# Kernel optimization log

Measured on AMD Instinct MI355X. Metric: run time of the kernel, lower is better.

The kernel has to match this reference:

```python
import jax, jax.numpy as jnp
import numpy as np

N_NODES = 50000
N_EDGES = 400000
IN, HID, OUT = 256, 64, 64
HEADS = (8, 8, 1)
NEG_SLOPE = 0.2


def setup_inputs() -> dict:
    key = jax.random.key(0)
    ks = jax.random.split(key, 16)
    def lin(k, fi, fo):
        return jax.random.normal(k, (fi, fo), jnp.float32) / np.sqrt(fi)
    H0, H1, H2 = HEADS
    return {
        "x": jax.random.normal(ks[0], (N_NODES, IN), jnp.float32),
        "src": jax.random.randint(ks[1], (N_EDGES,), 0, N_NODES),
        "dst": jax.random.randint(ks[2], (N_EDGES,), 0, N_NODES),
        # layer 0: in=256 -> (8 heads, 64)
        "W1": lin(ks[3], IN, H0 * HID),
        "al1": 0.1 * jax.random.normal(ks[4], (H0, HID), jnp.float32),
        "ar1": 0.1 * jax.random.normal(ks[5], (H0, HID), jnp.float32),
        "b1": jnp.zeros((H0 * HID,), jnp.float32),
        # layer 1: in=512 -> (8 heads, 64), identity residual (512 == 8*64)
        "W2": lin(ks[6], H0 * HID, H1 * HID),
        "al2": 0.1 * jax.random.normal(ks[7], (H1, HID), jnp.float32),
        "ar2": 0.1 * jax.random.normal(ks[8], (H1, HID), jnp.float32),
        "b2": jnp.zeros((H1 * HID,), jnp.float32),
        # layer 2: in=512 -> (1 head, 64), linear residual projection
        "W3": lin(ks[9], H1 * HID, H2 * OUT),
        "al3": 0.1 * jax.random.normal(ks[10], (H2, OUT), jnp.float32),
        "ar3": 0.1 * jax.random.normal(ks[11], (H2, OUT), jnp.float32),
        "b3": jnp.zeros((H2 * OUT,), jnp.float32),
        "Wr3": lin(ks[12], H1 * HID, H2 * OUT),
    }


def _gat_conv(h, src, dst, W, al, ar, b, res, act):
    # DGL GATConv on a homogeneous graph (feat_src == feat_dst).
    N = h.shape[0]
    H, D = al.shape
    f = (h @ W).reshape(N, H, D)                       # [N,H,D]
    el = jnp.sum(f * al[None], axis=-1)                # [N,H]
    er = jnp.sum(f * ar[None], axis=-1)                # [N,H]
    e = jax.nn.leaky_relu(el[src] + er[dst], NEG_SLOPE)  # [E,H]
    # segment softmax over incoming edges of each dst node
    m = jax.ops.segment_max(e, dst, num_segments=N)    # [N,H]
    ex = jnp.exp(e - m[dst])
    denom = jax.ops.segment_sum(ex, dst, num_segments=N)
    alpha = ex / denom[dst]                            # [E,H]
    msg = f[src] * alpha[:, :, None]                   # [E,H,D]
    rst = jax.ops.segment_sum(msg, dst, num_segments=N)  # [N,H,D]
    if res is not None:
        rst = rst + res
    rst = rst + b.reshape(1, H, D)
    return act(rst) if act is not None else rst


def reference(x, src, dst, W1, al1, ar1, b1, W2, al2, ar2, b2,
              W3, al3, ar3, b3, Wr3):
    N = x.shape[0]
    h = _gat_conv(x, src, dst, W1, al1, ar1, b1, None, jax.nn.elu)
    h = h.reshape(N, -1)                               # flatten(1)
    res2 = h.reshape(N, HEADS[1], HID)                 # identity residual
    h = _gat_conv(h, src, dst, W2, al2, ar2, b2, res2, jax.nn.elu)
    h = h.reshape(N, -1)
    res3 = (h @ Wr3).reshape(N, HEADS[2], OUT)         # projected residual
    h = _gat_conv(h, src, dst, W3, al3, ar3, b3, res3, None)
    return h.mean(axis=1)                              # mean over heads
```

## Files before the change

kernel.cpp:

```cpp
#include <hip/hip_runtime.h>
#include <hip/hip_bf16.h>

#define N_NODES 50000
#define M_PAD 50048
#define N_EDGES 400000
#define SCAN_B 256

typedef __attribute__((ext_vector_type(8))) short short8;
typedef __attribute__((ext_vector_type(4))) float f32x4;

__device__ __forceinline__ float b2f(unsigned short u) {
    return __uint_as_float(((unsigned)u) << 16);
}
__device__ __forceinline__ unsigned short f2b(float f) {
    unsigned u = __float_as_uint(f);
    return (unsigned short)((u + 0x7fffu + ((u >> 16) & 1u)) >> 16);
}
__device__ __forceinline__ float blo(unsigned u) { return __uint_as_float(u << 16); }
__device__ __forceinline__ float bhi(unsigned u) { return __uint_as_float(u & 0xffff0000u); }

__device__ __forceinline__ void gload_lds16(const void* g, void* l) {
    __builtin_amdgcn_global_load_lds(
        (const __attribute__((address_space(1))) unsigned int*)g,
        (__attribute__((address_space(3))) unsigned int*)l, 16, 0, 0);
}

__global__ __launch_bounds__(256) void conv_x4(const float* __restrict__ x,
                                               unsigned short* __restrict__ xb, int n4) {
    int i = blockIdx.x * blockDim.x + threadIdx.x;
    if (i >= n4) return;
    float4 v = *(const float4*)&x[(size_t)i * 4];
    unsigned short o[4] = {f2b(v.x), f2b(v.y), f2b(v.z), f2b(v.w)};
    *(ushort2*)&xb[(size_t)i * 4] = make_ushort2(o[0], o[1]);
    *(ushort2*)&xb[(size_t)i * 4 + 2] = make_ushort2(o[2], o[3]);
}

#define W1_SZ (512 * 256)
#define W2_SZ (512 * 512)
#define W3_SZ (64 * 512)
__global__ __launch_bounds__(256) void conv_wt_all(const float* __restrict__ W1,
                                                   const float* __restrict__ W2,
                                                   const float* __restrict__ W3,
                                                   const float* __restrict__ Wr3,
                                                   unsigned short* __restrict__ Wt1,
                                                   unsigned short* __restrict__ Wt2,
                                                   unsigned short* __restrict__ Wt3) {
    int o = blockIdx.x * blockDim.x + threadIdx.x;
    if (o < W1_SZ) {
        int n = o / 256, k = o % 256;
        Wt1[o] = f2b(W1[(size_t)k * 512 + n]);
    } else if (o < W1_SZ + W2_SZ) {
        int oo = o - W1_SZ;
        int n = oo / 512, k = oo % 512;
        Wt2[oo] = f2b(W2[(size_t)k * 512 + n]);
    } else if (o < W1_SZ + W2_SZ + W3_SZ) {
        int oo = o - W1_SZ - W2_SZ;
        int n = oo / 512, k = oo % 512;
        Wt3[oo] = f2b(W3[(size_t)k * 64 + n]);
    } else if (o < W1_SZ + W2_SZ + 2 * W3_SZ) {
        int oo = o - W1_SZ - W2_SZ - W3_SZ;
        int n = oo / 512, k = oo % 512;
        Wt3[W3_SZ + oo] = f2b(Wr3[(size_t)k * 64 + n]);
    }
}

template <int H, bool ELER>
__global__ __launch_bounds__(256, 2) void gemm_mfma(const unsigned short* __restrict__ A,
                                                    const unsigned short* __restrict__ Bt,
                                                    unsigned short* __restrict__ C,
                                                    const float* __restrict__ al,
                                                    const float* __restrict__ ar,
                                                    float* __restrict__ el,
                                                    float* __restrict__ er,
                                                    int M, int NN, int K) {
    __shared__ unsigned short As[128 * 32];
    __shared__ unsigned short Bs[128 * 32];
    const int tid = threadIdx.x;
    const int w = tid >> 6, l = tid & 63;
    const int bm = blockIdx.y * 128, bn = blockIdx.x * 128;
    const int wr = w >> 1, wc = w & 1;
    const int rA = l >> 2;
    const int kA = (l & 3) * 8;
    const int fr = l & 15, fq = l >> 4;
    f32x4 acc[4][4] = {};

    for (int k0 = 0; k0 < K; k0 += 32) {
#pragma unroll
        for (int j = 0; j < 2; ++j) {
            int row = w * 32 + j * 16 + rA;
            gload_lds16(&A[(size_t)(bm + row) * K + k0 + kA], &As[(w * 2 + j) * 512]);
            gload_lds16(&Bt[(size_t)(bn + row) * K + k0 + kA], &Bs[(w * 2 + j) * 512]);
        }
        __syncthreads();
        short8 a[4], b[4];
#pragma unroll
        for (int m = 0; m < 4; ++m)
            a[m] = *(const short8*)&As[(wr * 64 + m * 16 + fr) * 32 + fq * 8];
#pragma unroll
        for (int n = 0; n < 4; ++n)
            b[n] = *(const short8*)&Bs[(wc * 64 + n * 16 + fr) * 32 + fq * 8];
#pragma unroll
        for (int m = 0; m < 4; ++m)
#pragma unroll
            for (int n = 0; n < 4; ++n)
                acc[m][n] = __builtin_amdgcn_mfma_f32_16x16x32_bf16(a[m], b[n], acc[m][n], 0, 0, 0);
        __syncthreads();
    }

    if (ELER) {
        const int head = (bn >> 6) + wc;
        if (head < H) {
            float alv[4], arv[4];
#pragma unroll
            for (int n = 0; n < 4; ++n) {
                alv[n] = al[head * 64 + n * 16 + fr];
                arv[n] = ar[head * 64 + n * 16 + fr];
            }
#pragma unroll
            for (int m = 0; m < 4; ++m) {
#pragma unroll
                for (int j = 0; j < 4; ++j) {
                    float pl = acc[m][0][j] * alv[0] + acc[m][1][j] * alv[1] +
                               acc[m][2][j] * alv[2] + acc[m][3][j] * alv[3];
                    float pr = acc[m][0][j] * arv[0] + acc[m][1][j] * arv[1] +
                               acc[m][2][j] * arv[2] + acc[m][3][j] * arv[3];
#pragma unroll
                    for (int off = 1; off < 16; off <<= 1) {
                        pl += __shfl_xor(pl, off);
                        pr += __shfl_xor(pr, off);
                    }
                    int r = bm + wr * 64 + m * 16 + fq * 4 + j;
                    if (fr == 0 && r < M) {
                        el[(size_t)r * H + head] = pl;
                        er[(size_t)r * H + head] = pr;
                    }
                }
            }
        }
    }

#pragma unroll
    for (int m = 0; m < 4; ++m) {
#pragma unroll
        for (int j = 0; j < 4; ++j) {
            int r = bm + wr * 64 + m * 16 + fq * 4 + j;
            if (r < M) {
#pragma unroll
                for (int n = 0; n < 4; ++n)
                    C[(size_t)r * NN + bn + wc * 64 + n * 16 + fr] = f2b(acc[m][n][j]);
            }
        }
    }
}

__global__ __launch_bounds__(256) void hist_k(const int* __restrict__ dst,
                                              int* __restrict__ deg, int E) {
    int i = blockIdx.x * blockDim.x + threadIdx.x;
    if (i < E) atomicAdd(&deg[dst[i]], 1);
}

__global__ __launch_bounds__(SCAN_B) void scan_blocks(const int* __restrict__ in,
                                                      int* __restrict__ out,
                                                      int* __restrict__ part, int n) {
    __shared__ int tmp[SCAN_B];
    int t = threadIdx.x, g = blockIdx.x * SCAN_B + t;
    int v = (g < n) ? in[g] : 0;
    tmp[t] = v;
    __syncthreads();
    for (int off = 1; off < SCAN_B; off <<= 1) {
        int add = (t >= off) ? tmp[t - off] : 0;
        __syncthreads();
        tmp[t] += add;
        __syncthreads();
    }
    if (g < n) out[g] = tmp[t] - v;
    if (t == SCAN_B - 1) part[blockIdx.x] = tmp[t];
}

__global__ __launch_bounds__(SCAN_B) void scan_part(int* __restrict__ part, int n) {
    __shared__ int tmp[SCAN_B];
    int t = threadIdx.x;
    int v = (t < n) ? part[t] : 0;
    tmp[t] = v;
    __syncthreads();
    for (int off = 1; off < SCAN_B; off <<= 1) {
        int add = (t >= off) ? tmp[t - off] : 0;
        __syncthreads();
        tmp[t] += add;
        __syncthreads();
    }
    if (t < n) part[t] = tmp[t] - v;
}

__global__ __launch_bounds__(256) void add_off(int* __restrict__ rowptr,
                                               int* __restrict__ cursor,
                                               const int* __restrict__ part,
                                               int n, int E) {
    int g = blockIdx.x * blockDim.x + threadIdx.x;
    if (g < n) {
        int v = rowptr[g] + part[g / SCAN_B];
        rowptr[g] = v;
        cursor[g] = v;
    }
    if (g == 0) rowptr[n] = E;
}

__global__ __launch_bounds__(256) void scatter_k(const int* __restrict__ src,
                                                 const int* __restrict__ dst,
                                                 int* __restrict__ cursor,
                                                 int* __restrict__ csr_src, int E) {
    int e = blockIdx.x * blockDim.x + threadIdx.x;
    if (e < E) {
        int p = atomicAdd(&cursor[dst[e]], 1);
        csr_src[p] = src[e];
    }
}

template <bool HAS_INIT>
__global__ __launch_bounds__(256) void gat_agg8(const unsigned short* __restrict__ f,
                                                const float* __restrict__ el,
                                                const float* __restrict__ er,
                                                const int* __restrict__ rowptr,
                                                const int* __restrict__ csr_src,
                                                const unsigned short* __restrict__ init,
                                                const float* __restrict__ bias,
                                                unsigned short* __restrict__ outb, int N) {
    int w = (blockIdx.x * blockDim.x + threadIdx.x) >> 6;
    int lane = threadIdx.x & 63;
    if (w >= N) return;
    const int d = w;
    const int s0 = rowptr[d], s1 = rowptr[d + 1];
    const int hh = lane & 7;
    const int esub = lane >> 3;
    const float erh = er[(size_t)d * 8 + hh];

    float mx = -1e30f;
    for (int i = s0 + esub; i < s1; i += 8) {
        float v = el[(size_t)csr_src[i] * 8 + hh] + erh;
        v = v > 0.f ? v : 0.2f * v;
        mx = fmaxf(mx, v);
    }
#pragma unroll
    for (int off = 8; off < 64; off <<= 1) mx = fmaxf(mx, __shfl_xor(mx, off));

    float sm = 0.f;
    for (int i = s0 + esub; i < s1; i += 8) {
        float v = el[(size_t)csr_src[i] * 8 + hh] + erh;
        v = v > 0.f ? v : 0.2f * v;
        sm += __expf(v - mx);
    }
#pragma unroll
    for (int off = 8; off < 64; off <<= 1) sm += __shfl_xor(sm, off);
    const float inv = sm > 0.f ? 1.0f / sm : 0.f;

    const int myhead = lane >> 3;
    const int sl8 = lane * 8;
    float acc[8] = {};
    for (int i0 = s0; i0 < s1; i0 += 8) {
        int i = i0 + esub;
        bool valid = i < s1;
        int sn_mine = csr_src[valid ? i : s0];
        float v = el[(size_t)sn_mine * 8 + hh] + erh;
        v = v > 0.f ? v : 0.2f * v;
        float am = valid ? __expf(v - mx) * inv : 0.f;
#pragma unroll
        for (int j = 0; j < 8; ++j) {
            if (i0 + j >= s1) break;
            float alpha = __shfl(am, (j << 3) | myhead);
            int sn = __shfl(sn_mine, j << 3);
            uint4 pk = *(const uint4*)&f[(size_t)sn * 512 + sl8];
            acc[0] += blo(pk.x) * alpha;
            acc[1] += bhi(pk.x) * alpha;
            acc[2] += blo(pk.y) * alpha;
            acc[3] += bhi(pk.y) * alpha;
            acc[4] += blo(pk.z) * alpha;
            acc[5] += bhi(pk.z) * alpha;
            acc[6] += blo(pk.w) * alpha;
            acc[7] += bhi(pk.w) * alpha;
        }
    }

    const int sl = (lane & 7) * 8;
    float4 b0 = *(const float4*)&bias[myhead * 64 + sl];
    float4 b1 = *(const float4*)&bias[myhead * 64 + sl + 4];
    float bb[8] = {b0.x, b0.y, b0.z, b0.w, b1.x, b1.y, b1.z, b1.w};
    if (HAS_INIT) {
        uint4 iv = *(const uint4*)&init[(size_t)d * 512 + sl8];
        acc[0] += blo(iv.x); acc[1] += bhi(iv.x);
        acc[2] += blo(iv.y); acc[3] += bhi(iv.y);
        acc[4] += blo(iv.z); acc[5] += bhi(iv.z);
        acc[6] += blo(iv.w); acc[7] += bhi(iv.w);
    }
    unsigned short ob[8];
#pragma unroll
    for (int j = 0; j < 8; ++j) {
        float v = acc[j] + bb[j];
        v = v > 0.f ? v : __expf(v) - 1.f;
        ob[j] = f2b(v);
    }
    uint4 ov;
    ov.x = (unsigned)ob[0] | ((unsigned)ob[1] << 16);
    ov.y = (unsigned)ob[2] | ((unsigned)ob[3] << 16);
    ov.z = (unsigned)ob[4] | ((unsigned)ob[5] << 16);
    ov.w = (unsigned)ob[6] | ((unsigned)ob[7] << 16);
    *(uint4*)&outb[(size_t)d * 512 + sl8] = ov;
}

__global__ __launch_bounds__(256) void gat_agg1(const unsigned short* __restrict__ f,
                                                const float* __restrict__ el,
                                                const float* __restrict__ er,
                                                const int* __restrict__ rowptr,
                                                const int* __restrict__ csr_src,
                                                const float* __restrict__ bias,
                                                float* __restrict__ outf, int N) {
    int w = (blockIdx.x * blockDim.x + threadIdx.x) >> 6;
    int lane = threadIdx.x & 63;
    if (w >= N) return;
    const int d = w;
    const int s0 = rowptr[d], s1 = rowptr[d + 1];
    const float erh = er[d];

    float mx = -1e30f;
    for (int i = s0 + lane; i < s1; i += 64) {
        float v = el[csr_src[i]] + erh;
        v = v > 0.f ? v : 0.2f * v;
        mx = fmaxf(mx, v);
    }
#pragma unroll
    for (int off = 1; off < 64; off <<= 1) mx = fmaxf(mx, __shfl_xor(mx, off));

    float sm = 0.f;
    for (int i = s0 + lane; i < s1; i += 64) {
        float v = el[csr_src[i]] + erh;
        v = v > 0.f ? v : 0.2f * v;
        sm += __expf(v - mx);
    }
#pragma unroll
    for (int off = 1; off < 64; off <<= 1) sm += __shfl_xor(sm, off);
    const float inv = sm > 0.f ? 1.0f / sm : 0.f;

    const int esub = lane >> 3, sl = (lane & 7) * 8;
    float acc[8] = {};
    for (int i0 = s0; i0 < s1; i0 += 8) {
        int i = i0 + esub;
        bool valid = i < s1;
        int sn = csr_src[valid ? i : s0];
        float v = el[sn] + erh;
        v = v > 0.f ? v : 0.2f * v;
        float alpha = valid ? __expf(v - mx) * inv : 0.f;
        uint4 pk = *(const uint4*)&f[(size_t)sn * 128 + sl];
        acc[0] += blo(pk.x) * alpha;
        acc[1] += bhi(pk.x) * alpha;
        acc[2] += blo(pk.y) * alpha;
        acc[3] += bhi(pk.y) * alpha;
        acc[4] += blo(pk.z) * alpha;
        acc[5] += bhi(pk.z) * alpha;
        acc[6] += blo(pk.w) * alpha;
        acc[7] += bhi(pk.w) * alpha;
    }
#pragma unroll
    for (int off = 8; off < 64; off <<= 1)
#pragma unroll
        for (int j = 0; j < 8; ++j) acc[j] += __shfl_xor(acc[j], off);

    if (esub == 0) {
        uint4 rv = *(const uint4*)&f[(size_t)d * 128 + 64 + sl];
        float rr[8] = {blo(rv.x), bhi(rv.x), blo(rv.y), bhi(rv.y),
                       blo(rv.z), bhi(rv.z), blo(rv.w), bhi(rv.w)};
#pragma unroll
        for (int j = 0; j < 8; ++j)
            outf[(size_t)d * 64 + sl + j] = acc[j] + bias[sl + j] + rr[j];
    }
}

extern "C" void kernel_launch(void* const* d_in, const int* in_sizes, int n_in,
                              void* d_out, int out_size, void* d_ws, size_t ws_size,
                              hipStream_t stream) {
    const float* x   = (const float*)d_in[0];
    const int*   src = (const int*)d_in[1];
    const int*   dst = (const int*)d_in[2];
    const float* W1  = (const float*)d_in[3];
    const float* al1 = (const float*)d_in[4];
    const float* ar1 = (const float*)d_in[5];
    const float* b1  = (const float*)d_in[6];
    const float* W2  = (const float*)d_in[7];
    const float* al2 = (const float*)d_in[8];
    const float* ar2 = (const float*)d_in[9];
    const float* b2  = (const float*)d_in[10];
    const float* W3  = (const float*)d_in[11];
    const float* al3 = (const float*)d_in[12];
    const float* ar3 = (const float*)d_in[13];
    const float* b3  = (const float*)d_in[14];
    const float* Wr3 = (const float*)d_in[15];
    float* out = (float*)d_out;

    unsigned short* xb   = (unsigned short*)d_ws;
    unsigned short* fb   = xb + (size_t)M_PAD * 256;
    unsigned short* h1b  = fb + (size_t)M_PAD * 512;
    unsigned short* h2b  = h1b + (size_t)M_PAD * 512;
    unsigned short* f3r  = h2b + (size_t)M_PAD * 512;
    unsigned short* Wt1  = f3r + (size_t)M_PAD * 128;
    unsigned short* Wt2  = Wt1 + 512 * 256;
    unsigned short* Wt3  = Wt2 + 512 * 512;
    float* el = (float*)(Wt3 + 128 * 512);
    float* er = el + (size_t)N_NODES * 8;
    int* rowptr  = (int*)(er + (size_t)N_NODES * 8);
    int* cursor  = rowptr + (N_NODES + 1);
    int* part    = cursor + N_NODES;
    int* csr_src = part + 256;

    const dim3 blk(256);
    const int E = N_EDGES, N = N_NODES;
    const int nb = (N + SCAN_B - 1) / SCAN_B;
    const int gy = (N + 127) / 128;

    conv_x4<<<(N * 64 + 255) / 256, blk, 0, stream>>>(x, xb, N * 64);
    conv_wt_all<<<(W1_SZ + W2_SZ + 2 * W3_SZ + 255) / 256, blk, 0, stream>>>(
        W1, W2, W3, Wr3, Wt1, Wt2, Wt3);

    hipMemsetAsync(cursor, 0, (size_t)N * 4, stream);
    hist_k<<<(E + 255) / 256, blk, 0, stream>>>(dst, cursor, E);
    scan_blocks<<<nb, SCAN_B, 0, stream>>>(cursor, rowptr, part, N);
    scan_part<<<1, SCAN_B, 0, stream>>>(part, nb);
    add_off<<<nb, blk, 0, stream>>>(rowptr, cursor, part, N, E);
    scatter_k<<<(E + 255) / 256, blk, 0, stream>>>(src, dst, cursor, csr_src, E);

    gemm_mfma<8, true><<<dim3(4, gy), blk, 0, stream>>>(
        xb, Wt1, fb, al1, ar1, el, er, N, 512, 256);
    gat_agg8<false><<<(N + 3) / 4, blk, 0, stream>>>(
        fb, el, er, rowptr, csr_src, nullptr, b1, h1b, N);

    gemm_mfma<8, true><<<dim3(4, gy), blk, 0, stream>>>(
        h1b, Wt2, fb, al2, ar2, el, er, N, 512, 512);
    gat_agg8<true><<<(N + 3) / 4, blk, 0, stream>>>(
        fb, el, er, rowptr, csr_src, h1b, b2, h2b, N);

    gemm_mfma<1, true><<<dim3(1, gy), blk, 0, stream>>>(
        h2b, Wt3, f3r, al3, ar3, el, er, N, 128, 512);
    gat_agg1<<<(N + 3) / 4, blk, 0, stream>>>(
        f3r, el, er, rowptr, csr_src, b3, out, N);
}
```

Before: 369.6 us.

## Fuse softmax sum into aggregation pass and prefetch first edge batch

The aggregation kernels now fold the softmax denominator into the weighted accumulation pass and normalise at the end, which removes the separate sum pass over edges. gat_agg8 also issues the feature gathers for a whole batch of eight edges before using them, and the first batch is loaded before the max pass so its latency overlaps that pass. The x and weight conversion kernels are merged into one launch. A pad of zeros after csr_src keeps the unconditional batch loads in bounds, at the cost of more live registers.

```diff
diff --git a/kernel.cpp b/kernel.cpp
--- a/kernel.cpp
+++ b/kernel.cpp
@@ -25,27 +25,28 @@
         (__attribute__((address_space(3))) unsigned int*)l, 16, 0, 0);
 }
 
-__global__ __launch_bounds__(256) void conv_x4(const float* __restrict__ x,
-                                               unsigned short* __restrict__ xb, int n4) {
-    int i = blockIdx.x * blockDim.x + threadIdx.x;
-    if (i >= n4) return;
-    float4 v = *(const float4*)&x[(size_t)i * 4];
-    unsigned short o[4] = {f2b(v.x), f2b(v.y), f2b(v.z), f2b(v.w)};
-    *(ushort2*)&xb[(size_t)i * 4] = make_ushort2(o[0], o[1]);
-    *(ushort2*)&xb[(size_t)i * 4 + 2] = make_ushort2(o[2], o[3]);
-}
-
+#define X4_N (N_NODES * 64)
 #define W1_SZ (512 * 256)
 #define W2_SZ (512 * 512)
 #define W3_SZ (64 * 512)
-__global__ __launch_bounds__(256) void conv_wt_all(const float* __restrict__ W1,
-                                                   const float* __restrict__ W2,
-                                                   const float* __restrict__ W3,
-                                                   const float* __restrict__ Wr3,
-                                                   unsigned short* __restrict__ Wt1,
-                                                   unsigned short* __restrict__ Wt2,
-                                                   unsigned short* __restrict__ Wt3) {
-    int o = blockIdx.x * blockDim.x + threadIdx.x;
+__global__ __launch_bounds__(256) void prep_k(const float* __restrict__ x,
+                                              const float* __restrict__ W1,
+                                              const float* __restrict__ W2,
+                                              const float* __restrict__ W3,
+                                              const float* __restrict__ Wr3,
+                                              unsigned short* __restrict__ xb,
+                                              unsigned short* __restrict__ Wt1,
+                                              unsigned short* __restrict__ Wt2,
+                                              unsigned short* __restrict__ Wt3) {
+    int i = blockIdx.x * blockDim.x + threadIdx.x;
+    if (i < X4_N) {
+        float4 v = *(const float4*)&x[(size_t)i * 4];
+        unsigned short o[4] = {f2b(v.x), f2b(v.y), f2b(v.z), f2b(v.w)};
+        *(ushort2*)&xb[(size_t)i * 4] = make_ushort2(o[0], o[1]);
+        *(ushort2*)&xb[(size_t)i * 4 + 2] = make_ushort2(o[2], o[3]);
+        return;
+    }
+    int o = i - X4_N;
     if (o < W1_SZ) {
         int n = o / 256, k = o % 256;
         Wt1[o] = f2b(W1[(size_t)k * 512 + n]);
@@ -232,53 +233,83 @@
     const int s0 = rowptr[d], s1 = rowptr[d + 1];
     const int hh = lane & 7;
     const int esub = lane >> 3;
+    const int myhead = lane >> 3;
+    const int sl8 = lane * 8;
     const float erh = er[(size_t)d * 8 + hh];
 
-    float mx = -1e30f;
-    for (int i = s0 + esub; i < s1; i += 8) {
+    int i0 = s0 + esub;
+    bool valid0 = i0 < s1;
+    int sn0 = csr_src[valid0 ? i0 : s0];
+    uint4 pk[8];
+#pragma unroll
+    for (int j = 0; j < 8; ++j) {
+        int snj = __shfl(sn0, j << 3);
+        pk[j] = *(const uint4*)&f[(size_t)snj * 512 + sl8];
+    }
+
+    float v0 = el[(size_t)sn0 * 8 + hh] + erh;
+    v0 = v0 > 0.f ? v0 : 0.2f * v0;
+    float mx = valid0 ? v0 : -1e30f;
+    for (int i = s0 + 8 + esub; i < s1; i += 8) {
         float v = el[(size_t)csr_src[i] * 8 + hh] + erh;
         v = v > 0.f ? v : 0.2f * v;
         mx = fmaxf(mx, v);
     }
-#pragma unroll
-    for (int off = 8; off < 64; off <<= 1) mx = fmaxf(mx, __shfl_xor(mx, off));
-
-    float sm = 0.f;
-    for (int i = s0 + esub; i < s1; i += 8) {
-        float v = el[(size_t)csr_src[i] * 8 + hh] + erh;
-        v = v > 0.f ? v : 0.2f * v;
-        sm += __expf(v - mx);
-    }
-#pragma unroll
-    for (int off = 8; off < 64; off <<= 1) sm += __shfl_xor(sm, off);
-    const float inv = sm > 0.f ? 1.0f / sm : 0.f;
-
-    const int myhead = lane >> 3;
-    const int sl8 = lane * 8;
+    mx = fmaxf(mx, __shfl_xor(mx, 8));
+    mx = fmaxf(mx, __shfl_xor(mx, 16));
+    mx = fmaxf(mx, __shfl_xor(mx, 32));
+
+    float am0 = valid0 ? __expf(v0 - mx) : 0.f;
+    float sm = am0;
     float acc[8] = {};
-    for (int i0 = s0; i0 < s1; i0 += 8) {
-        int i = i0 + esub;
+#pragma unroll
+    for (int j = 0; j < 8; ++j) {
+        float alpha = __shfl(am0, (j << 3) | myhead);
+        acc[0] += blo(pk[j].x) * alpha;
+        acc[1] += bhi(pk[j].x) * alpha;
+        acc[2] += blo(pk[j].y) * alpha;
+        acc[3] += bhi(pk[j].y) * alpha;
+        acc[4] += blo(pk[j].z) * alpha;
+        acc[5] += bhi(pk[j].z) * alpha;
+        acc[6] += blo(pk[j].w) * alpha;
+        acc[7] += bhi(pk[j].w) * alpha;
+    }
+
+    for (int ii = s0 + 8; ii < s1; ii += 8) {
+        int i = ii + esub;
         bool valid = i < s1;
         int sn_mine = csr_src[valid ? i : s0];
+        uint4 qk[8];
+#pragma unroll
+        for (int j = 0; j < 8; ++j) {
+            int snj = __shfl(sn_mine, j << 3);
+            qk[j] = *(const uint4*)&f[(size_t)snj * 512 + sl8];
+        }
         float v = el[(size_t)sn_mine * 8 + hh] + erh;
         v = v > 0.f ? v : 0.2f * v;
-        float am = valid ? __expf(v - mx) * inv : 0.f;
+        float am = valid ? __expf(v - mx) : 0.f;
+        sm += am;
 #pragma unroll
         for (int j = 0; j < 8; ++j) {
-            if (i0 + j >= s1) break;
             float alpha = __shfl(am, (j << 3) | myhead);
-            int sn = __shfl(sn_mine, j << 3);
-            uint4 pk = *(const uint4*)&f[(size_t)sn * 512 + sl8];
-            acc[0] += blo(pk.x) * alpha;
-            acc[1] += bhi(pk.x) * alpha;
-            acc[2] += blo(pk.y) * alpha;
-            acc[3] += bhi(pk.y) * alpha;
-            acc[4] += blo(pk.z) * alpha;
-            acc[5] += bhi(pk.z) * alpha;
-            acc[6] += blo(pk.w) * alpha;
-            acc[7] += bhi(pk.w) * alpha;
+            acc[0] += blo(qk[j].x) * alpha;
+            acc[1] += bhi(qk[j].x) * alpha;
+            acc[2] += blo(qk[j].y) * alpha;
+            acc[3] += bhi(qk[j].y) * alpha;
+            acc[4] += blo(qk[j].z) * alpha;
+            acc[5] += bhi(qk[j].z) * alpha;
+            acc[6] += blo(qk[j].w) * alpha;
+            acc[7] += bhi(qk[j].w) * alpha;
         }
     }
+
+    sm += __shfl_xor(sm, 8);
+    sm += __shfl_xor(sm, 16);
+    sm += __shfl_xor(sm, 32);
+    float smh = __shfl(sm, myhead);
+    float inv = smh > 0.f ? 1.0f / smh : 0.f;
+#pragma unroll
+    for (int j = 0; j < 8; ++j) acc[j] *= inv;
 
     const int sl = (lane & 7) * 8;
     float4 b0 = *(const float4*)&bias[myhead * 64 + sl];
@@ -318,50 +349,57 @@
     if (w >= N) return;
     const int d = w;
     const int s0 = rowptr[d], s1 = rowptr[d + 1];
+    const int esub = lane >> 3, sl = (lane & 7) * 8;
     const float erh = er[d];
 
-    float mx = -1e30f;
-    for (int i = s0 + lane; i < s1; i += 64) {
+    int i0 = s0 + esub;
+    bool valid0 = i0 < s1;
+    int sn0 = csr_src[valid0 ? i0 : s0];
+    uint4 pk0 = *(const uint4*)&f[(size_t)sn0 * 128 + sl];
+
+    float v0 = el[sn0] + erh;
+    v0 = v0 > 0.f ? v0 : 0.2f * v0;
+    float mx = valid0 ? v0 : -1e30f;
+    for (int i = s0 + 8 + esub; i < s1; i += 8) {
         float v = el[csr_src[i]] + erh;
         v = v > 0.f ? v : 0.2f * v;
         mx = fmaxf(mx, v);
     }
-#pragma unroll
-    for (int off = 1; off < 64; off <<= 1) mx = fmaxf(mx, __shfl_xor(mx, off));
-
-    float sm = 0.f;
-    for (int i = s0 + lane; i < s1; i += 64) {
-        float v = el[csr_src[i]] + erh;
-        v = v > 0.f ? v : 0.2f * v;
-        sm += __expf(v - mx);
-    }
-#pragma unroll
-    for (int off = 1; off < 64; off <<= 1) sm += __shfl_xor(sm, off);
-    const float inv = sm > 0.f ? 1.0f / sm : 0.f;
-
-    const int esub = lane >> 3, sl = (lane & 7) * 8;
-    float acc[8] = {};
-    for (int i0 = s0; i0 < s1; i0 += 8) {
-        int i = i0 + esub;
+    mx = fmaxf(mx, __shfl_xor(mx, 8));
+    mx = fmaxf(mx, __shfl_xor(mx, 16));
+    mx = fmaxf(mx, __shfl_xor(mx, 32));
+
+    float am0 = valid0 ? __expf(v0 - mx) : 0.f;
+    float sm = am0;
+    float acc[8];
+    acc[0] = blo(pk0.x) * am0; acc[1] = bhi(pk0.x) * am0;
+    acc[2] = blo(pk0.y) * am0; acc[3] = bhi(pk0.y) * am0;
+    acc[4] = blo(pk0.z) * am0; acc[5] = bhi(pk0.z) * am0;
+    acc[6] = blo(pk0.w) * am0; acc[7] = bhi(pk0.w) * am0;
+
+    for (int ii = s0 + 8; ii < s1; ii += 8) {
+        int i = ii + esub;
         bool valid = i < s1;
         int sn = csr_src[valid ? i : s0];
+        uint4 pk = *(const uint4*)&f[(size_t)sn * 128 + sl];
         float v = el[sn] + erh;
         v = v > 0.f ? v : 0.2f * v;
-        float alpha = valid ? __expf(v - mx) * inv : 0.f;
-        uint4 pk = *(const uint4*)&f[(size_t)sn * 128 + sl];
-        acc[0] += blo(pk.x) * alpha;
-        acc[1] += bhi(pk.x) * alpha;
-        acc[2] += blo(pk.y) * alpha;
-        acc[3] += bhi(pk.y) * alpha;
-        acc[4] += blo(pk.z) * alpha;
-        acc[5] += bhi(pk.z) * alpha;
-        acc[6] += blo(pk.w) * alpha;
-        acc[7] += bhi(pk.w) * alpha;
-    }
+        float am = valid ? __expf(v - mx) : 0.f;
+        sm += am;
+        acc[0] += blo(pk.x) * am; acc[1] += bhi(pk.x) * am;
+        acc[2] += blo(pk.y) * am; acc[3] += bhi(pk.y) * am;
+        acc[4] += blo(pk.z) * am; acc[5] += bhi(pk.z) * am;
+        acc[6] += blo(pk.w) * am; acc[7] += bhi(pk.w) * am;
+    }
+
+    sm += __shfl_xor(sm, 8);
+    sm += __shfl_xor(sm, 16);
+    sm += __shfl_xor(sm, 32);
 #pragma unroll
     for (int off = 8; off < 64; off <<= 1)
 #pragma unroll
         for (int j = 0; j < 8; ++j) acc[j] += __shfl_xor(acc[j], off);
+    float inv = sm > 0.f ? 1.0f / sm : 0.f;
 
     if (esub == 0) {
         uint4 rv = *(const uint4*)&f[(size_t)d * 128 + 64 + sl];
@@ -369,7 +407,7 @@
                        blo(rv.z), bhi(rv.z), blo(rv.w), bhi(rv.w)};
 #pragma unroll
         for (int j = 0; j < 8; ++j)
-            outf[(size_t)d * 64 + sl + j] = acc[j] + bias[sl + j] + rr[j];
+            outf[(size_t)d * 64 + sl + j] = acc[j] * inv + bias[sl + j] + rr[j];
     }
 }
 
@@ -414,11 +452,11 @@
     const int nb = (N + SCAN_B - 1) / SCAN_B;
     const int gy = (N + 127) / 128;
 
-    conv_x4<<<(N * 64 + 255) / 256, blk, 0, stream>>>(x, xb, N * 64);
-    conv_wt_all<<<(W1_SZ + W2_SZ + 2 * W3_SZ + 255) / 256, blk, 0, stream>>>(
-        W1, W2, W3, Wr3, Wt1, Wt2, Wt3);
+    prep_k<<<(X4_N + W1_SZ + W2_SZ + 2 * W3_SZ + 255) / 256, blk, 0, stream>>>(
+        x, W1, W2, W3, Wr3, xb, Wt1, Wt2, Wt3);
 
     hipMemsetAsync(cursor, 0, (size_t)N * 4, stream);
+    hipMemsetAsync(csr_src + E, 0, 8 * 4, stream);
     hist_k<<<(E + 255) / 256, blk, 0, stream>>>(dst, cursor, E);
     scan_blocks<<<nb, SCAN_B, 0, stream>>>(cursor, rowptr, part, N);
     scan_part<<<1, SCAN_B, 0, stream>>>(part, nb);
```

Result: faster. 357.0 us (-3.4%).
